# Kernel optimization log

Hardware: AMD Instinct MI355X
Metric: run time of the kernel (lower is better)

The kernel has to match this reference:

```python
import jax, jax.numpy as jnp
import numpy as np

N_COMP = 5
EPS = 0.1
BATCH = 2_097_152
BISECT_ITERS = 60
LAM_HI = 1e6  # upper bracket for the KL-constraint Lagrange multiplier


def setup_inputs() -> dict:
    key = jax.random.key(0)
    kx, kw, kb = jax.random.split(key, 3)
    # Positive inputs/weights keep q = x @ W.T + b > 0 (cp.kl_div domain).
    x = jax.random.uniform(kx, (BATCH, N_COMP), dtype=jnp.float32)
    W = jax.random.uniform(kw, (N_COMP, N_COMP), dtype=jnp.float32) * 0.5
    b = jax.random.uniform(kb, (N_COMP,), dtype=jnp.float32) * 0.5 + 0.1
    return {"x": x, "W": W, "b": b}


def _kl_ball_project(q, eps):
    """Solve min_p sum(kl_div(p,q)) s.t. sum(kl_div(p,r)) <= eps, sum(p)=1, p>=0
    with r = uniform (the module's first-call r_prev = ones/n, sum(r)=1).

    With sum(p)=1 the extra (-p + q) / (-p + r) terms of cp.kl_div are constants,
    so this is min KL(p||q) s.t. KL(p||r) <= eps on the simplex. KKT gives the
    closed-form geometric-mixture path p(lam) ~ q^{1/(1+lam)} * r^{lam/(1+lam)};
    we bisect on lam >= 0 to hit KL(p||r) = eps (lam=0 if already feasible).
    """
    n = q.shape[-1]
    logq = jnp.log(q)                                   # [B, n]
    log_r = -jnp.log(jnp.float32(n))                    # uniform r

    def p_of(lam, lq):
        t = (1.0 / (1.0 + lam))[..., None]              # [B, 1]
        return jax.nn.softmax(t * lq + (1.0 - t) * log_r, axis=-1)

    def g(lam, lq):  # constraint residual KL(p(lam) || r) - eps, shape [B]
        p = p_of(lam, lq)
        return jnp.sum(p * (jnp.log(p) - log_r), axis=-1) - eps

    # Bisection on a stop-gradient copy: lam is treated as a constant w.r.t. q
    # (envelope-style), so no solver iterations are stored for autodiff.
    lq_sg = jax.lax.stop_gradient(logq)
    zeros = jnp.zeros(q.shape[:-1], q.dtype)
    g0 = g(zeros, lq_sg)                                # feasibility at lam=0

    def body(carry, _):
        lo, hi = carry
        mid = 0.5 * (lo + hi)
        gm = g(mid, lq_sg)
        lo = jnp.where(gm > 0, mid, lo)
        hi = jnp.where(gm > 0, hi, mid)
        return (lo, hi), None

    (lo, hi), _ = jax.lax.scan(body, (zeros, jnp.full_like(zeros, LAM_HI)),
                               None, length=BISECT_ITERS)
    lam = jnp.where(g0 <= 0, 0.0, 0.5 * (lo + hi))      # exact 0 if feasible
    return p_of(lam, logq)


def reference(x, W, b):
    q = x @ W.T + b                                     # nn.Linear
    return _kl_ball_project(q, EPS)
```

## Files before the change

kernel.cpp:

```cpp
#include <hip/hip_runtime.h>
#include <math.h>

#define NC 5
#define EPS_F 0.1f

__device__ __forceinline__ float frcp(float v) { return __builtin_amdgcn_rcpf(v); }

__global__ __launch_bounds__(256) void klproj_kernel(
    const float* __restrict__ x,
    const float* __restrict__ W,
    const float* __restrict__ b,
    float* __restrict__ out,
    int half)
{
    int i = blockIdx.x * blockDim.x + threadIdx.x;
    if (i >= half) return;

    const float C = 1.6094379124341003f - EPS_F;

    float u[2][NC], u2[2][NC], t[2], lo[2], hi[2], f1[2];

#pragma unroll
    for (int r = 0; r < 2; ++r) {
        int row = i + r * half;
        float xv[NC];
#pragma unroll
        for (int k = 0; k < NC; ++k) xv[k] = x[row * NC + k];
        float s[NC];
        float m = -1e30f;
#pragma unroll
        for (int j = 0; j < NC; ++j) {
            float q = b[j];
#pragma unroll
            for (int k = 0; k < NC; ++k) q = fmaf(xv[k], W[j * NC + k], q);
            s[j] = __logf(q);
            m = fmaxf(m, s[j]);
        }
#pragma unroll
        for (int j = 0; j < NC; ++j) {
            u[r][j]  = s[j] - m;
            u2[r][j] = u[r][j] * u[r][j];
        }
    }

    auto eval = [&](int r, float tt, float& f, float& fp) {
        float Z = 0.f, T1 = 0.f, T2 = 0.f;
#pragma unroll
        for (int j = 0; j < NC; ++j) {
            float ej = __expf(tt * u[r][j]);
            Z += ej;
            T1 = fmaf(ej, u[r][j], T1);
            T2 = fmaf(ej, u2[r][j], T2);
        }
        float rZ = frcp(Z);
        float Eu = T1 * rZ;
        f  = fmaf(tt, Eu, C - __logf(Z));
        fp = tt * fmaf(-Eu, Eu, T2 * rZ);
    };

    bool any = false;
#pragma unroll
    for (int r = 0; r < 2; ++r) {
        float fp1;
        eval(r, 1.0f, f1[r], fp1);
        lo[r] = 0.f; hi[r] = 1.f;
        float kl1 = f1[r] + EPS_F;
        float t0  = 0.316227766017f * __frsqrt_rn(kl1);
        t[r] = (t0 > 0.f && t0 < 1.f) ? t0 : 0.5f;
        any = any || (f1[r] > 0.f);
    }

    if (any) {
#pragma unroll
        for (int it = 0; it < 6; ++it) {
#pragma unroll
            for (int r = 0; r < 2; ++r) {
                float f, fp;
                eval(r, t[r], f, fp);
                bool pos = f > 0.f;
                hi[r] = pos ? t[r] : hi[r];
                lo[r] = pos ? lo[r] : t[r];
                float tn = t[r] - f * frcp(fp);
                t[r] = (tn > lo[r] && tn < hi[r]) ? tn : 0.5f * (lo[r] + hi[r]);
            }
        }
    }

#pragma unroll
    for (int r = 0; r < 2; ++r) {
        float tf = (f1[r] > 0.f) ? t[r] : 1.0f;
        float e[NC], Z = 0.f;
#pragma unroll
        for (int j = 0; j < NC; ++j) { e[j] = __expf(tf * u[r][j]); Z += e[j]; }
        float rZ = frcp(Z);
        int row = i + r * half;
#pragma unroll
        for (int j = 0; j < NC; ++j) out[row * NC + j] = e[j] * rZ;
    }
}

extern "C" void kernel_launch(void* const* d_in, const int* in_sizes, int n_in,
                              void* d_out, int out_size, void* d_ws, size_t ws_size,
                              hipStream_t stream) {
    const float* x = (const float*)d_in[0];
    const float* W = (const float*)d_in[1];
    const float* b = (const float*)d_in[2];
    float* out = (float*)d_out;
    int batch = in_sizes[0] / NC;
    int half = batch / 2;

    int block = 256;
    int grid = (half + block - 1) / block;
    klproj_kernel<<<grid, block, 0, stream>>>(x, W, b, out, half);
}
```

Measured before the change: 95.97 us.

## Process four contiguous rows per thread with float4 vectorized loads and stores

Each thread now handles four consecutive rows (20 floats) and moves them with five float4 loads and five float4 stores, replacing the scalar strided accesses to two rows half a batch apart. The rows' outputs are written back into the same registers before storing. The u^2 array is dropped and recomputed inside eval, which saves registers. This targets memory transaction efficiency and adds more independent Newton chains per thread for ILP, at the cost of higher register pressure, half as many threads, and a silent assumption that the batch is divisible by four.

```diff
diff --git a/kernel.cpp b/kernel.cpp
--- a/kernel.cpp
+++ b/kernel.cpp
@@ -3,54 +3,40 @@
 
 #define NC 5
 #define EPS_F 0.1f
+#define RPT 4
 
 __device__ __forceinline__ float frcp(float v) { return __builtin_amdgcn_rcpf(v); }
 
 __global__ __launch_bounds__(256) void klproj_kernel(
-    const float* __restrict__ x,
+    const float4* __restrict__ x4,
     const float* __restrict__ W,
     const float* __restrict__ b,
-    float* __restrict__ out,
-    int half)
+    float4* __restrict__ out4,
+    int nthreads)
 {
     int i = blockIdx.x * blockDim.x + threadIdx.x;
-    if (i >= half) return;
+    if (i >= nthreads) return;
+
+    float4 L[5];
+#pragma unroll
+    for (int k = 0; k < 5; ++k) L[k] = x4[i * 5 + k];
+    float* v = (float*)L;
 
     const float C = 1.6094379124341003f - EPS_F;
 
-    float u[2][NC], u2[2][NC], t[2], lo[2], hi[2], f1[2];
-
-#pragma unroll
-    for (int r = 0; r < 2; ++r) {
-        int row = i + r * half;
-        float xv[NC];
-#pragma unroll
-        for (int k = 0; k < NC; ++k) xv[k] = x[row * NC + k];
-        float s[NC];
-        float m = -1e30f;
-#pragma unroll
-        for (int j = 0; j < NC; ++j) {
-            float q = b[j];
-#pragma unroll
-            for (int k = 0; k < NC; ++k) q = fmaf(xv[k], W[j * NC + k], q);
-            s[j] = __logf(q);
-            m = fmaxf(m, s[j]);
-        }
-#pragma unroll
-        for (int j = 0; j < NC; ++j) {
-            u[r][j]  = s[j] - m;
-            u2[r][j] = u[r][j] * u[r][j];
-        }
-    }
+    float u[RPT][NC], t[RPT], lo[RPT], hi[RPT];
+    bool infeas[RPT];
 
     auto eval = [&](int r, float tt, float& f, float& fp) {
         float Z = 0.f, T1 = 0.f, T2 = 0.f;
 #pragma unroll
         for (int j = 0; j < NC; ++j) {
-            float ej = __expf(tt * u[r][j]);
+            float uj = u[r][j];
+            float ej = __expf(tt * uj);
+            float eu = ej * uj;
             Z += ej;
-            T1 = fmaf(ej, u[r][j], T1);
-            T2 = fmaf(ej, u2[r][j], T2);
+            T1 += eu;
+            T2 = fmaf(eu, uj, T2);
         }
         float rZ = frcp(Z);
         float Eu = T1 * rZ;
@@ -60,21 +46,33 @@
 
     bool any = false;
 #pragma unroll
-    for (int r = 0; r < 2; ++r) {
-        float fp1;
-        eval(r, 1.0f, f1[r], fp1);
+    for (int r = 0; r < RPT; ++r) {
+        float s[NC], m = -1e30f;
+#pragma unroll
+        for (int j = 0; j < NC; ++j) {
+            float q = b[j];
+#pragma unroll
+            for (int k = 0; k < NC; ++k) q = fmaf(v[r * NC + k], W[j * NC + k], q);
+            s[j] = __logf(q);
+            m = fmaxf(m, s[j]);
+        }
+#pragma unroll
+        for (int j = 0; j < NC; ++j) u[r][j] = s[j] - m;
+
+        float f1, fp1;
+        eval(r, 1.0f, f1, fp1);
+        infeas[r] = (f1 > 0.f);
         lo[r] = 0.f; hi[r] = 1.f;
-        float kl1 = f1[r] + EPS_F;
-        float t0  = 0.316227766017f * __frsqrt_rn(kl1);
+        float t0 = 0.316227766017f * __frsqrt_rn(f1 + EPS_F);
         t[r] = (t0 > 0.f && t0 < 1.f) ? t0 : 0.5f;
-        any = any || (f1[r] > 0.f);
+        any = any || infeas[r];
     }
 
     if (any) {
 #pragma unroll
         for (int it = 0; it < 6; ++it) {
 #pragma unroll
-            for (int r = 0; r < 2; ++r) {
+            for (int r = 0; r < RPT; ++r) {
                 float f, fp;
                 eval(r, t[r], f, fp);
                 bool pos = f > 0.f;
@@ -87,16 +85,18 @@
     }
 
 #pragma unroll
-    for (int r = 0; r < 2; ++r) {
-        float tf = (f1[r] > 0.f) ? t[r] : 1.0f;
+    for (int r = 0; r < RPT; ++r) {
+        float tf = infeas[r] ? t[r] : 1.0f;
         float e[NC], Z = 0.f;
 #pragma unroll
         for (int j = 0; j < NC; ++j) { e[j] = __expf(tf * u[r][j]); Z += e[j]; }
         float rZ = frcp(Z);
-        int row = i + r * half;
 #pragma unroll
-        for (int j = 0; j < NC; ++j) out[row * NC + j] = e[j] * rZ;
+        for (int j = 0; j < NC; ++j) v[r * NC + j] = e[j] * rZ;
     }
+
+#pragma unroll
+    for (int k = 0; k < 5; ++k) out4[i * 5 + k] = L[k];
 }
 
 extern "C" void kernel_launch(void* const* d_in, const int* in_sizes, int n_in,
@@ -107,9 +107,10 @@
     const float* b = (const float*)d_in[2];
     float* out = (float*)d_out;
     int batch = in_sizes[0] / NC;
-    int half = batch / 2;
+    int nthreads = batch / RPT;
 
     int block = 256;
-    int grid = (half + block - 1) / block;
-    klproj_kernel<<<grid, block, 0, stream>>>(x, W, b, out, half);
+    int grid = (nthreads + block - 1) / block;
+    klproj_kernel<<<grid, block, 0, stream>>>(
+        (const float4*)x, W, b, (float4*)out, nthreads);
 }
```

Measured after the change: 98.89 us. +3.0%, slower.
